# Performance work log

Hardware: AMD Instinct MI355X
Metric: run time of the kernel (lower is better)

The kernel has to match this reference:

```python
import jax, jax.numpy as jnp
import numpy as np

# Module hyperparameters (from init_kwargs)
IN_C = 64
OUT_C = 64
K = 3
STRIDE = 1
PAD = 1
DIL = 1
OVERLAP = 4
CENTER_SIZE = 4

# Input sizes
B, H, W = 16, 128, 128


def _crop_mask(h, w):
    """Static (trace-time) crop mask: zeros on the central crop window, ones elsewhere.

    Matches the intended semantics of CropConv's python-loop mask: rows
    [crop_start, crop_start+crop_size) x cols [crop_start, crop_start+crop_size)
    of the HxW output grid are zeroed.
    """
    crop_start = (h - h // CENTER_SIZE) // 2 - OVERLAP  # 44 for h=128
    crop_size = h // CENTER_SIZE + 2 * OVERLAP          # 40 for h=128
    m = np.ones((h, w), dtype=np.float32)
    m[crop_start:crop_start + crop_size, crop_start:crop_start + crop_size] = 0.0
    return jnp.asarray(m)


def setup_inputs() -> dict:
    key = jax.random.key(0)
    kx, kw = jax.random.split(key)
    x = jax.random.normal(kx, (B, IN_C, H, W), dtype=jnp.float32)
    # kaiming_normal_ fan_out init: std = sqrt(2 / (out_channels * k * k))
    w_std = np.sqrt(2.0 / (OUT_C * K * K)).astype(np.float32)
    weight = jax.random.normal(kw, (OUT_C, IN_C, K, K), dtype=jnp.float32) * w_std
    return {"x": x, "weight": weight}


def reference(x, weight):
    # im2col (Unfold) + matmul == a standard dense conv; use the fused conv primitive.
    out = jax.lax.conv_general_dilated(
        x, weight,
        window_strides=(STRIDE, STRIDE),
        padding=((PAD, PAD), (PAD, PAD)),
        rhs_dilation=(DIL, DIL),
        dimension_numbers=("NCHW", "OIHW", "NCHW"),
    )  # [B, OUT_C, H, W] (same-size conv)
    mask = _crop_mask(out.shape[2], out.shape[3])  # [H, W], {0,1}
    # torch.where(mask, out, 0) == out * mask (mask is constant wrt grads)
    return out * mask
```

## Files before the change

### kernel.cpp

```cpp
#include <hip/hip_runtime.h>
#include <stdint.h>


#define B_ 16
#define C_ 64
#define H_ 128
#define W_ 128

#define WLDS_U4 4608
#define XLDS_U4 4096

typedef float f32x4 __attribute__((ext_vector_type(4)));
typedef short bf16x8 __attribute__((ext_vector_type(8)));

__device__ inline unsigned short f2bf(float f) {
    union { float f; uint32_t u; } v; v.f = f;
    uint32_t u = v.u + 0x7FFF + ((v.u >> 16) & 1);
    return (unsigned short)(u >> 16);
}

__global__ __launch_bounds__(256, 1) void conv_fused(
    const float* __restrict__ x,
    const float* __restrict__ wgt,
    float* __restrict__ out)
{
    __shared__ uint4 lds[WLDS_U4 + XLDS_U4];
    uint16_t* lds16 = (uint16_t*)lds;

    const int t    = threadIdx.x;
    const int lane = t & 63;
    const int wv   = t >> 6;
    const int n    = lane & 15;
    const int q    = lane >> 4;

    const int d    = blockIdx.x;
    const int orig = (d & 7) * 128 + (d >> 3);
    const int b    = orig >> 6;
    const int h0   = (orig & 63) * 2;

    #pragma unroll
    for (int p = 0; p < 2; ++p) {
        const int a_  = t + 256 * p;
        const int oc  = a_ >> 3;
        const int oct = a_ & 7;
        const float* src = wgt + (size_t)oc * 576 + (size_t)oct * 72;
        f32x4 w4[18];
        #pragma unroll
        for (int j = 0; j < 18; ++j) w4[j] = ((const f32x4*)src)[j];
        const int ch = oct >> 2, qq = oct & 3;
        const int ii = oc >> 4,  nn = oc & 15;
        #pragma unroll
        for (int kk = 0; kk < 9; ++kk) {
            #define WELEM(e) ((uint32_t)f2bf(w4[((e)*9 + kk) >> 2][((e)*9 + kk) & 3]))
            uint4 val;
            val.x = WELEM(0) | (WELEM(1) << 16);
            val.y = WELEM(2) | (WELEM(3) << 16);
            val.z = WELEM(4) | (WELEM(5) << 16);
            val.w = WELEM(6) | (WELEM(7) << 16);
            #undef WELEM
            lds[((kk * 2 + ch) * 4 + ii) * 64 + qq * 16 + nn] = val;
        }
    }

    {
        const int ic    = t >> 2;
        const int w0    = (t & 3) * 32;
        const int jslot = ic >> 3;
        const int esub  = ic & 7;
        #pragma unroll
        for (int r = 0; r < 4; ++r) {
            const int h = h0 - 1 + r;
            if (h < 0 || h >= H_) {
                uint4 z; z.x = z.y = z.z = z.w = 0;
                #pragma unroll
                for (int k = 0; k < 4; ++k)
                    lds[WLDS_U4 + r * 1024 + k * 256 + t] = z;
            } else {
                const float* src =
                    x + (((size_t)(b * C_ + ic)) * H_ + h) * W_ + w0;
                f32x4 v4[8];
                #pragma unroll
                for (int j = 0; j < 8; ++j) v4[j] = ((const f32x4*)src)[j];
                #pragma unroll
                for (int k = 0; k < 32; ++k) {
                    const int c    = w0 + k;
                    const int slot = (jslot + c) & 7;
                    lds16[WLDS_U4 * 8 + ((r * 128 + c) * 8 + slot) * 8 + esub] =
                        f2bf(v4[k >> 2][k & 3]);
                }
            }
        }
    }
    __syncthreads();

    f32x4 acc[4][4];
    #pragma unroll
    for (int i = 0; i < 4; ++i)
        #pragma unroll
        for (int tt = 0; tt < 4; ++tt)
            acc[i][tt] = (f32x4){0.f, 0.f, 0.f, 0.f};

    const int wb = (wv & 1) * 64;
    const uint4* Wl = lds;
    const uint4* Xl = lds + WLDS_U4;
    const bool lz = (wb + n) == 0;
    const bool rz = (wb + n) == 79;
    const bf16x8 zfrag = 0;

    #pragma unroll
    for (int kh = 0; kh < 3; ++kh) {
        const int row = (wv >> 1) + kh;
        #pragma unroll
        for (int kw = 0; kw < 3; ++kw) {
            const int kk = kh * 3 + kw;
            #pragma unroll
            for (int ch = 0; ch < 2; ++ch) {
                bf16x8 a[4], bb[4];
                #pragma unroll
                for (int i = 0; i < 4; ++i)
                    a[i] = __builtin_bit_cast(bf16x8,
                        Wl[((kk * 2 + ch) * 4 + i) * 64 + lane]);
                #pragma unroll
                for (int tt = 0; tt < 4; ++tt) {
                    int c   = wb + tt * 16 + n + kw - 1;
                    int cc  = min(max(c, 0), 127);
                    int idx = (row * 128 + cc) * 8 + ((ch * 4 + q + cc) & 7);
                    bf16x8 v = __builtin_bit_cast(bf16x8, Xl[idx]);
                    if (kw == 0 && tt == 0) v = lz ? zfrag : v;
                    if (kw == 2 && tt == 3) v = rz ? zfrag : v;
                    bb[tt] = v;
                }
                #pragma unroll
                for (int i = 0; i < 4; ++i)
                    #pragma unroll
                    for (int tt = 0; tt < 4; ++tt)
                        acc[i][tt] = __builtin_amdgcn_mfma_f32_16x16x32_bf16(
                            a[i], bb[tt], acc[i][tt], 0, 0, 0);
            }
        }
    }

    const int  h  = h0 + (wv >> 1);
    const bool hz = (h >= 44 && h < 84);
    #pragma unroll
    for (int i = 0; i < 4; ++i) {
        #pragma unroll
        for (int tt = 0; tt < 4; ++tt) {
            const int  w0 = wb + tt * 16 + n;
            const bool zz = hz && (w0 >= 44 && w0 < 84);
            #pragma unroll
            for (int r = 0; r < 4; ++r) {
                const int oc = i * 16 + q * 4 + r;
                out[(((size_t)b * C_ + oc) * H_ + h) * W_ + w0] =
                    zz ? 0.f : acc[i][tt][r];
            }
        }
    }
}

extern "C" void kernel_launch(void* const* d_in, const int* in_sizes, int n_in,
                              void* d_out, int out_size, void* d_ws, size_t ws_size,
                              hipStream_t stream) {
    const float* x   = (const float*)d_in[0];
    const float* wgt = (const float*)d_in[1];
    float* out       = (float*)d_out;
    (void)d_ws; (void)ws_size;
    conv_fused<<<dim3(1024), dim3(256), 0, stream>>>(x, wgt, out);
}
```

Baseline: 140.8 us.

## Pre-transform weights to bf16 in workspace and read them from global memory

Adds a small kernel that converts the weights once per call into the MFMA fragment layout in bf16 and stores them in the workspace. The main conv kernel then loads A fragments straight from global memory (cached in L2/L1) instead of every block redoing the weight conversion into LDS. This cuts LDS use to the input tile, which allows two blocks per CU. The x staging is also reworked so threads read coalesced along width across channels. The cost is an extra kernel launch, plus global or cache loads of weights inside the inner loop.

```diff
diff --git a/kernel.cpp b/kernel.cpp
--- a/kernel.cpp
+++ b/kernel.cpp
@@ -7,7 +7,6 @@
 #define H_ 128
 #define W_ 128
 
-#define WLDS_U4 4608
 #define XLDS_U4 4096
 
 typedef float f32x4 __attribute__((ext_vector_type(4)));
@@ -18,6 +17,134 @@
     uint32_t u = v.u + 0x7FFF + ((v.u >> 16) & 1);
     return (unsigned short)(u >> 16);
 }
+
+__global__ __launch_bounds__(256) void xform_weight(
+    const float* __restrict__ wgt, uint16_t* __restrict__ Wb)
+{
+    int L = blockIdx.x * 256 + threadIdx.x;
+    int e    = L & 7;
+    int lane = (L >> 3) & 63;
+    int i    = (L >> 9) & 3;
+    int ch   = (L >> 11) & 1;
+    int kk   = L >> 12;
+    int oc   = i * 16 + (lane & 15);
+    int ic   = ch * 32 + (lane >> 4) * 8 + e;
+    Wb[L] = f2bf(wgt[((size_t)oc * 64 + ic) * 9 + kk]);
+}
+
+__global__ __launch_bounds__(256, 2) void conv_main(
+    const uint4* __restrict__ Wq,
+    const float* __restrict__ x,
+    float* __restrict__ out)
+{
+    __shared__ uint4 lds[XLDS_U4];
+
+    const int t    = threadIdx.x;
+    const int lane = t & 63;
+    const int wv   = t >> 6;
+    const int n    = lane & 15;
+    const int q    = lane >> 4;
+
+    const int d    = blockIdx.x;
+    const int orig = (d & 7) * 128 + (d >> 3);
+    const int b    = orig >> 6;
+    const int h0   = (orig & 63) * 2;
+
+    {
+        const int c     = t & 127;
+        const int jbase = (t >> 7) * 4;
+        #pragma unroll
+        for (int r = 0; r < 4; ++r) {
+            const int h = h0 - 1 + r;
+            if (h < 0 || h >= H_) {
+                uint4 z; z.x = z.y = z.z = z.w = 0;
+                #pragma unroll
+                for (int jj = 0; jj < 4; ++jj)
+                    lds[r * 1024 + c * 8 + ((jbase + jj + c) & 7)] = z;
+            } else {
+                const float* src = x + (((size_t)b * C_) * H_ + h) * W_ + c;
+                #pragma unroll
+                for (int jj = 0; jj < 4; ++jj) {
+                    const int j = jbase + jj;
+                    uint32_t u[4];
+                    #pragma unroll
+                    for (int p = 0; p < 4; ++p) {
+                        float v0 = src[(size_t)(j * 8 + 2 * p)     * (H_ * W_)];
+                        float v1 = src[(size_t)(j * 8 + 2 * p + 1) * (H_ * W_)];
+                        u[p] = (uint32_t)f2bf(v0) | ((uint32_t)f2bf(v1) << 16);
+                    }
+                    lds[r * 1024 + c * 8 + ((j + c) & 7)] =
+                        *(const uint4*)u;
+                }
+            }
+        }
+    }
+    __syncthreads();
+
+    f32x4 acc[4][4];
+    #pragma unroll
+    for (int i = 0; i < 4; ++i)
+        #pragma unroll
+        for (int tt = 0; tt < 4; ++tt)
+            acc[i][tt] = (f32x4){0.f, 0.f, 0.f, 0.f};
+
+    const int wb = (wv & 1) * 64;
+    const bool lz = (wb + n) == 0;
+    const bool rz = (wb + n) == 79;
+    const bf16x8 zfrag = 0;
+
+    #pragma unroll
+    for (int kh = 0; kh < 3; ++kh) {
+        const int row = (wv >> 1) + kh;
+        #pragma unroll
+        for (int kw = 0; kw < 3; ++kw) {
+            const int kk = kh * 3 + kw;
+            #pragma unroll
+            for (int ch = 0; ch < 2; ++ch) {
+                bf16x8 a[4], bb[4];
+                #pragma unroll
+                for (int i = 0; i < 4; ++i)
+                    a[i] = __builtin_bit_cast(bf16x8,
+                        Wq[((kk * 2 + ch) * 4 + i) * 64 + lane]);
+                #pragma unroll
+                for (int tt = 0; tt < 4; ++tt) {
+                    int c   = wb + tt * 16 + n + kw - 1;
+                    int cc  = min(max(c, 0), 127);
+                    int idx = (row * 128 + cc) * 8 + ((ch * 4 + q + cc) & 7);
+                    bf16x8 v = __builtin_bit_cast(bf16x8, lds[idx]);
+                    if (kw == 0 && tt == 0) v = lz ? zfrag : v;
+                    if (kw == 2 && tt == 3) v = rz ? zfrag : v;
+                    bb[tt] = v;
+                }
+                #pragma unroll
+                for (int i = 0; i < 4; ++i)
+                    #pragma unroll
+                    for (int tt = 0; tt < 4; ++tt)
+                        acc[i][tt] = __builtin_amdgcn_mfma_f32_16x16x32_bf16(
+                            a[i], bb[tt], acc[i][tt], 0, 0, 0);
+            }
+        }
+    }
+
+    const int  h  = h0 + (wv >> 1);
+    const bool hz = (h >= 44 && h < 84);
+    #pragma unroll
+    for (int i = 0; i < 4; ++i) {
+        #pragma unroll
+        for (int tt = 0; tt < 4; ++tt) {
+            const int  w0 = wb + tt * 16 + n;
+            const bool zz = hz && (w0 >= 44 && w0 < 84);
+            #pragma unroll
+            for (int r = 0; r < 4; ++r) {
+                const int oc = i * 16 + q * 4 + r;
+                out[(((size_t)b * C_ + oc) * H_ + h) * W_ + w0] =
+                    zz ? 0.f : acc[i][tt][r];
+            }
+        }
+    }
+}
+
+#define WLDS_U4 4608
 
 __global__ __launch_bounds__(256, 1) void conv_fused(
     const float* __restrict__ x,
@@ -164,6 +291,14 @@
     const float* x   = (const float*)d_in[0];
     const float* wgt = (const float*)d_in[1];
     float* out       = (float*)d_out;
-    (void)d_ws; (void)ws_size;
-    conv_fused<<<dim3(1024), dim3(256), 0, stream>>>(x, wgt, out);
-}
+
+    const size_t W_BYTES = 9 * 2 * 4 * 64 * 16;
+    if (ws_size >= W_BYTES) {
+        uint16_t* Wb = (uint16_t*)d_ws;
+        xform_weight<<<dim3(144), dim3(256), 0, stream>>>(wgt, Wb);
+        conv_main<<<dim3(1024), dim3(256), 0, stream>>>(
+            (const uint4*)Wb, x, out);
+    } else {
+        conv_fused<<<dim3(1024), dim3(256), 0, stream>>>(x, wgt, out);
+    }
+}
```

New measurement: 132.5 us. 1.06x faster.
